# Performance work log

Measured on AMD Instinct MI355X. Metric: run time of the kernel, lower is better.

## Reference

```python
import jax, jax.numpy as jnp
import numpy as np

N = 50000
E = 500000
HID = 64
HEADS = 4
LAYERS = 4
CDIM = 8


def _p(key, shape, scale=0.05):
    return jax.random.normal(key, shape, dtype=jnp.float32) * scale


def setup_inputs() -> dict:
    key = jax.random.key(0)
    ks = jax.random.split(key, 32)
    x = jax.random.normal(ks[0], (N, 8), dtype=jnp.float32)
    src = jax.random.randint(ks[1], (E,), 0, N)
    dst = jax.random.randint(ks[2], (E,), 0, N)
    edge_index = jnp.stack([src, dst]).astype(jnp.int64)
    HC = HEADS * HID
    inp = {
        "x": x,
        "edge_index": edge_index,
        # encoder: Linear(8,64), ELU, Linear(64,64), ELU
        "enc_w1": _p(ks[3], (HID, 8)), "enc_b1": _p(ks[4], (HID,)),
        "enc_w2": _p(ks[5], (HID, HID)), "enc_b2": _p(ks[6], (HID,)),
        # per-layer TransformerConv params, stacked over layers
        "Wq": _p(ks[7], (LAYERS, HC, HID)), "bq": _p(ks[8], (LAYERS, HC)),
        "Wk": _p(ks[9], (LAYERS, HC, HID)), "bk": _p(ks[10], (LAYERS, HC)),
        "Wv": _p(ks[11], (LAYERS, HC, HID)), "bv": _p(ks[12], (LAYERS, HC)),
        "Ws": _p(ks[13], (LAYERS, HID, HID)), "bs": _p(ks[14], (LAYERS, HID)),
        # output MLP: 64->64->32->8
        "out_w1": _p(ks[15], (64, HID)), "out_b1": _p(ks[16], (64,)),
        "out_w2": _p(ks[17], (32, 64)), "out_b2": _p(ks[18], (32,)),
        "out_w3": _p(ks[19], (CDIM, 32)), "out_b3": _p(ks[20], (CDIM,)),
    }
    return inp


def transformer_conv(h, src, dst, Wq, bq, Wk, bk, Wv, bv, Ws, bs):
    """PyG TransformerConv, concat=False, root_weight=True, eval mode (no dropout)."""
    n = h.shape[0]
    q = (h @ Wq.T + bq).reshape(n, HEADS, HID)
    k = (h @ Wk.T + bk).reshape(n, HEADS, HID)
    v = (h @ Wv.T + bv).reshape(n, HEADS, HID)
    # per-edge multi-head scores: (E, H)
    alpha = jnp.einsum("ehd,ehd->eh", q[dst], k[src]) / np.sqrt(HID).astype(np.float32)
    # segment softmax over edges grouped by destination node
    amax = jax.ops.segment_max(alpha, dst, num_segments=n)          # (N, H)
    ex = jnp.exp(alpha - amax[dst])                                 # (E, H)
    denom = jax.ops.segment_sum(ex, dst, num_segments=n)           # (N, H)
    w = ex / denom[dst]                                             # (E, H)
    msg = v[src] * w[:, :, None]                                    # (E, H, C)
    agg = jax.ops.segment_sum(msg, dst, num_segments=n)            # (N, H, C)
    out = agg.mean(axis=1)                                          # concat=False -> head mean
    return out + h @ Ws.T + bs                                      # skip connection


def reference(x, edge_index, enc_w1, enc_b1, enc_w2, enc_b2,
              Wq, bq, Wk, bk, Wv, bv, Ws, bs,
              out_w1, out_b1, out_w2, out_b2, out_w3, out_b3):
    src, dst = edge_index[0], edge_index[1]
    elu = jax.nn.elu
    h = elu(x @ enc_w1.T + enc_b1)
    h = elu(h @ enc_w2.T + enc_b2)
    for l in range(LAYERS):
        h = elu(transformer_conv(h, src, dst, Wq[l], bq[l], Wk[l], bk[l],
                                 Wv[l], bv[l], Ws[l], bs[l]))
        # dropout is identity in eval mode
    o = elu(h @ out_w1.T + out_b1)
    o = elu(o @ out_w2.T + out_b2)
    o = o @ out_w3.T + out_b3
    return o
```

## Files before the change

kernel.cpp:

```cpp
#include <hip/hip_runtime.h>
#include <hip/hip_bf16.h>

#define N_NODES 50000
#define N_EDGES 500000
constexpr int HID = 64;
constexpr int HC  = 256;

typedef unsigned short u16;
typedef unsigned char u8;
typedef __attribute__((ext_vector_type(8))) __bf16 bf16x8;
typedef __attribute__((ext_vector_type(4))) float f32x4;
typedef __attribute__((ext_vector_type(2))) float f32x2;

__device__ __forceinline__ float b2f(u16 u) {
    union { unsigned int i; float f; } c; c.i = ((unsigned int)u) << 16; return c.f;
}
__device__ __forceinline__ u16 f2b(float f) {
    union { float f; unsigned int i; } c; c.f = f;
    unsigned int x = c.i;
    unsigned int lsb = (x >> 16) & 1u;
    x += 0x7fffu + lsb;
    return (u16)(x >> 16);
}
__device__ __forceinline__ float elu_f(float x) { return x > 0.f ? x : expm1f(x); }


__global__ __launch_bounds__(256) void init_kernel(int* __restrict__ cnt, int* __restrict__ cursor) {
    int i = blockIdx.x * 256 + threadIdx.x;
    if (i < N_NODES) { cnt[i] = 0; cursor[i] = 0; }
}

__global__ __launch_bounds__(256) void detect_kernel(const int* __restrict__ ei, int* __restrict__ flag) {
    __shared__ int s[4];
    int t = threadIdx.x;
    int nz = ei[2 * t + 1] != 0;
    unsigned long long m = __ballot(nz);
    if ((t & 63) == 0) s[t >> 6] = (m != 0ull) ? 1 : 0;
    __syncthreads();
    if (t == 0) flag[0] = s[0] | s[1] | s[2] | s[3];
}

__global__ __launch_bounds__(256) void hist_kernel(const int* __restrict__ ei, const int* __restrict__ flag,
                                                   int* __restrict__ cnt) {
    int e = blockIdx.x * 256 + threadIdx.x;
    if (e < N_EDGES) {
        int d = flag[0] ? ei[N_EDGES + e] : ei[2 * N_EDGES + 2 * e];
        atomicAdd(&cnt[d], 1);
    }
}

__global__ __launch_bounds__(512) void scan1_kernel(const int* __restrict__ cnt,
                                                    int* __restrict__ row_start, int* __restrict__ bsum) {
    __shared__ int sc[512];
    int t = threadIdx.x;
    int i = blockIdx.x * 512 + t;
    int v = (i < N_NODES) ? cnt[i] : 0;
    sc[t] = v;
    __syncthreads();
    for (int off = 1; off < 512; off <<= 1) {
        int u = (t >= off) ? sc[t - off] : 0;
        __syncthreads();
        sc[t] += u;
        __syncthreads();
    }
    if (i < N_NODES) row_start[i] = sc[t] - v;
    if (t == 511) bsum[blockIdx.x] = sc[511];
}

__global__ __launch_bounds__(128) void scan2_kernel(int* __restrict__ bsum, int* __restrict__ row_start) {
    __shared__ int sc[128];
    const int NB = (N_NODES + 511) / 512;
    int t = threadIdx.x;
    int v = (t < NB) ? bsum[t] : 0;
    sc[t] = v;
    __syncthreads();
    for (int off = 1; off < 128; off <<= 1) {
        int u = (t >= off) ? sc[t - off] : 0;
        __syncthreads();
        sc[t] += u;
        __syncthreads();
    }
    if (t < NB) bsum[t] = sc[t] - v;
    if (t == 127) row_start[N_NODES] = sc[127];
}

__global__ __launch_bounds__(512) void scan3_kernel(int* __restrict__ row_start, const int* __restrict__ bsum) {
    int i = blockIdx.x * 512 + threadIdx.x;
    if (i < N_NODES) row_start[i] += bsum[blockIdx.x];
}

__global__ __launch_bounds__(256) void scatter_kernel(const int* __restrict__ ei, const int* __restrict__ flag,
                                const int* __restrict__ row_start, int* __restrict__ cursor,
// ... 28 lines not shown
    }
    if (t >= 128 && t < 256) {
        int p = t - 128;
        int row = p >> 1, c = (p & 1) * 4;
        float4 val = *(const float4*)(w1 + row * 8 + c);
        *(float4*)&w1s[row * 9 + c] = val;
    }
    #pragma unroll
    for (int r = 0; r < 4; ++r) {
        int p = t + r * 256; int row = p >> 4, kc = (p & 15) * 4;
        float4 val = *(const float4*)(w2 + row * 64 + kc);
        ushort4 u; u.x = f2b(val.x); u.y = f2b(val.y); u.z = f2b(val.z); u.w = f2b(val.w);
        *(ushort4*)&w2s[row * 72 + kc] = u;
    }
    if (t < 64) { b1s[t] = b1[t]; b2s[t] = b2[t]; }
    __syncthreads();

    {
        int j = t & 63, sub = t >> 6;
        #pragma unroll
        for (int g = 0; g < 16; ++g) {
            int node = g * 4 + sub;
            float acc = b1s[j];
            #pragma unroll
            for (int m = 0; m < 8; ++m) acc += xs[node * 9 + m] * w1s[j * 9 + m];
            t1s[node * 72 + j] = f2b(elu_f(acc));
        }
    }
    __syncthreads();

    int wave = t >> 6, lane = t & 63;
    int lrow = lane & 15, quad = lane >> 4;
    int m_off = wave * 16;
    bf16x8 a0 = *(const bf16x8*)&t1s[(m_off + lrow) * 72 + quad * 8];
    bf16x8 a1 = *(const bf16x8*)&t1s[(m_off + lrow) * 72 + 32 + quad * 8];
    #pragma unroll
    for (int nsub = 0; nsub < 4; ++nsub) {
        bf16x8 b0 = *(const bf16x8*)&w2s[(nsub * 16 + lrow) * 72 + quad * 8];
        bf16x8 b1v = *(const bf16x8*)&w2s[(nsub * 16 + lrow) * 72 + 32 + quad * 8];
        f32x4 acc = {0.f, 0.f, 0.f, 0.f};
        acc = __builtin_amdgcn_mfma_f32_16x16x32_bf16(a0, b0, acc, 0, 0, 0);
        acc = __builtin_amdgcn_mfma_f32_16x16x32_bf16(a1, b1v, acc, 0, 0, 0);
        int col = nsub * 16 + lrow;
        float bias = b2s[col];
        #pragma unroll
        for (int r = 0; r < 4; ++r) {
            int row = m0 + m_off + quad * 4 + r;
            if (row < N_NODES) h[(size_t)row * 64 + col] = elu_f(acc[r] + bias);
        }
    }
}

__global__ __launch_bounds__(256) void proj_kernel(const float* __restrict__ h,
    const float* __restrict__ Wq, const float* __restrict__ bq,
    const float* __restrict__ Wk, const float* __restrict__ bk,
    const float* __restrict__ Wv, const float* __restrict__ bv,
    const float* __restrict__ Wsk, const float* __restrict__ bsk,
    int layer,
    u16* __restrict__ q, u8* __restrict__ kv,
    float* __restrict__ skip)
{
    __shared__ u16 as_tile[64 * 72];
    __shared__ u16 ws_tile[64 * 72];
    __shared__ float bias_s[64];
    __shared__ float stage[4][16 * 68];
    int t = threadIdx.x;
    int m0 = blockIdx.x * 64;

    #pragma unroll
    for (int r = 0; r < 4; ++r) {
        int p = t + r * 256; int row = p >> 4, kc = (p & 15) * 4;
        float4 val = make_float4(0.f, 0.f, 0.f, 0.f);
        if (m0 + row < N_NODES) val = *(const float4*)(h + (size_t)(m0 + row) * 64 + kc);
        ushort4 u; u.x = f2b(val.x); u.y = f2b(val.y); u.z = f2b(val.z); u.w = f2b(val.w);
        *(ushort4*)&as_tile[row * 72 + kc] = u;
    }
    __syncthreads();

    int wave = t >> 6, lane = t & 63;
    int lrow = lane & 15, quad = lane >> 4;
    int m_off = wave * 16;
    bf16x8 a0 = *(const bf16x8*)&as_tile[(m_off + lrow) * 72 + quad * 8];
    bf16x8 a1 = *(const bf16x8*)&as_tile[(m_off + lrow) * 72 + 32 + quad * 8];

    for (int ct = 0; ct < 13; ++ct) {
        const float *Wp, *bp; int cbase; int mode;
        if (ct < 4)       { Wp = Wq  + (size_t)layer * HC * HID;  bp = bq  + layer * HC;  cbase = ct * 64;       mode = 0; }
        else if (ct < 8)  { Wp = Wk  + (size_t)layer * HC * HID;  bp = bk  + layer * HC;  cbase = (ct - 4) * 64; mode = 1; }
        else if (ct < 12) { Wp = Wv  + (size_t)layer * HC * HID;  bp = bv  + layer * HC;  cbase = (ct - 8) * 64; mode = 2; }
        else              { Wp = Wsk + (size_t)layer * HID * HID; bp = bsk + layer * HID; cbase = 0;             mode = 3; }

        __syncthreads();
        #pragma unroll
        for (int r = 0; r < 4; ++r) {
            int p = t + r * 256; int row = p >> 4, kc = (p & 15) * 4;
            float4 val = *(const float4*)(Wp + (size_t)(cbase + row) * 64 + kc);
            ushort4 u; u.x = f2b(val.x); u.y = f2b(val.y); u.z = f2b(val.z); u.w = f2b(val.w);
            *(ushort4*)&ws_tile[row * 72 + kc] = u;
        }
        if (t < 64) bias_s[t] = bp[cbase + t];
        __syncthreads();

        if (mode == 1 || mode == 2) {
            #pragma unroll
            for (int nsub = 0; nsub < 4; ++nsub) {
                bf16x8 b0 = *(const bf16x8*)&ws_tile[(nsub * 16 + lrow) * 72 + quad * 8];
                bf16x8 b1 = *(const bf16x8*)&ws_tile[(nsub * 16 + lrow) * 72 + 32 + quad * 8];
                f32x4 acc = {0.f, 0.f, 0.f, 0.f};
                acc = __builtin_amdgcn_mfma_f32_16x16x32_bf16(a0, b0, acc, 0, 0, 0);
                acc = __builtin_amdgcn_mfma_f32_16x16x32_bf16(a1, b1, acc, 0, 0, 0);
                float bias = bias_s[nsub * 16 + lrow];
                #pragma unroll
                for (int r = 0; r < 4; ++r)
                    stage[wave][(quad * 4 + r) * 68 + nsub * 16 + lrow] = (acc[r] + bias) * 16.f;
            }
            int row_l = lane >> 2;
            int c0 = (lane & 3) * 16;
            int grow = m0 + m_off + row_l;
            if (grow < N_NODES) {
                const float* sp = &stage[wave][row_l * 68 + c0];
                u8* base = kv + (size_t)grow * 512 + (size_t)((cbase + c0) >> 2) * 8 + (mode == 1 ? 0 : 4);
                #pragma unroll
                for (int j = 0; j < 4; ++j) {
                    float f0 = sp[4 * j + 0], f1 = sp[4 * j + 1];
                    float f2v = sp[4 * j + 2], f3v = sp[4 * j + 3];
                    int pk = __builtin_amdgcn_cvt_pk_fp8_f32(f0, f1, 0, false);
                    pk = __builtin_amdgcn_cvt_pk_fp8_f32(f2v, f3v, pk, true);
                    *(int*)(base + j * 8) = pk;
                }
            }
        } else {
            #pragma unroll
            for (int nsub = 0; nsub < 4; ++nsub) {
                bf16x8 b0 = *(const bf16x8*)&ws_tile[(nsub * 16 + lrow) * 72 + quad * 8];
                bf16x8 b1 = *(const bf16x8*)&ws_tile[(nsub * 16 + lrow) * 72 + 32 + quad * 8];
                f32x4 acc = {0.f, 0.f, 0.f, 0.f};
                acc = __builtin_amdgcn_mfma_f32_16x16x32_bf16(a0, b0, acc, 0, 0, 0);
                acc = __builtin_amdgcn_mfma_f32_16x16x32_bf16(a1, b1, acc, 0, 0, 0);
                int col = cbase + nsub * 16 + lrow;
                float bias = bias_s[nsub * 16 + lrow];
                #pragma unroll
                for (int r = 0; r < 4; ++r) {
                    int row = m0 + m_off + quad * 4 + r;
                    if (row < N_NODES) {
                        float o = acc[r] + bias;
                        if (mode == 0) q[(size_t)row * 256 + col] = f2b(o);
                        else           skip[(size_t)row * 64 + col] = o;
                    }
                }
            }
        }
    }
}

__global__ __launch_bounds__(256) void attn_kernel(
    const u16* __restrict__ q, const u8* __restrict__ kv,
    const float* __restrict__ skip,
    const int* __restrict__ row_start, const int* __restrict__ csr_src,
    float* __restrict__ hout)
{
    int wave = threadIdx.x >> 6;
    int lane = threadIdx.x & 63;
    int n = blockIdx.x * 4 + wave;
    if (n >= N_NODES) return;
    ushort4 q4 = ((const ushort4*)(q + (size_t)n * 256))[lane];
    float qf0 = b2f(q4.x), qf1 = b2f(q4.y), qf2 = b2f(q4.z), qf3 = b2f(q4.w);
    float l = 0.f;
    float a0 = 0.f, a1 = 0.f, a2 = 0.f, a3 = 0.f;
    int e0 = row_start[n], e1 = row_start[n + 1];
    for (int e = e0; e < e1; e += 4) {
        int rem = e1 - e;
        int i1 = rem > 1 ? e + 1 : e;
        int i2 = rem > 2 ? e + 2 : e;
        int i3 = rem > 3 ? e + 3 : e;
        int s0 = csr_src[e], s1 = csr_src[i1], s2 = csr_src[i2], s3 = csr_src[i3];
        uint2 c0 = *(const uint2*)(kv + (size_t)s0 * 512 + lane * 8);
        uint2 c1 = *(const uint2*)(kv + (size_t)s1 * 512 + lane * 8);
        uint2 c2 = *(const uint2*)(kv + (size_t)s2 * 512 + lane * 8);
        uint2 c3 = *(const uint2*)(kv + (size_t)s3 * 512 + lane * 8);
        f32x2 k0a = __builtin_amdgcn_cvt_pk_f32_fp8(c0.x, false), k0b = __builtin_amdgcn_cvt_pk_f32_fp8(c0.x, true);
        f32x2 k1a = __builtin_amdgcn_cvt_pk_f32_fp8(c1.x, false), k1b = __builtin_amdgcn_cvt_pk_f32_fp8(c1.x, true);
        f32x2 k2a = __builtin_amdgcn_cvt_pk_f32_fp8(c2.x, false), k2b = __builtin_amdgcn_cvt_pk_f32_fp8(c2.x, true);
        f32x2 k3a = __builtin_amdgcn_cvt_pk_f32_fp8(c3.x, false), k3b = __builtin_amdgcn_cvt_pk_f32_fp8(c3.x, true);
        float p0 = qf0 * k0a.x + qf1 * k0a.y + qf2 * k0b.x + qf3 * k0b.y;
        float p1 = qf0 * k1a.x + qf1 * k1a.y + qf2 * k1b.x + qf3 * k1b.y;
        float p2 = qf0 * k2a.x + qf1 * k2a.y + qf2 * k2b.x + qf3 * k2b.y;
        float p3 = qf0 * k3a.x + qf1 * k3a.y + qf2 * k3b.x + qf3 * k3b.y;
        p0 += __shfl_xor(p0, 1); p1 += __shfl_xor(p1, 1); p2 += __shfl_xor(p2, 1); p3 += __shfl_xor(p3, 1);
        p0 += __shfl_xor(p0, 2); p1 += __shfl_xor(p1, 2); p2 += __shfl_xor(p2, 2); p3 += __shfl_xor(p3, 2);
        p0 += __shfl_xor(p0, 4); p1 += __shfl_xor(p1, 4); p2 += __shfl_xor(p2, 4); p3 += __shfl_xor(p3, 4);
        p0 += __shfl_xor(p0, 8); p1 += __shfl_xor(p1, 8); p2 += __shfl_xor(p2, 8); p3 += __shfl_xor(p3, 8);
        const float S = 0.0078125f;
        float w0 = __expf(p0 * S);
        float w1 = rem > 1 ? __expf(p1 * S) : 0.f;
        float w2 = rem > 2 ? __expf(p2 * S) : 0.f;
        float w3 = rem > 3 ? __expf(p3 * S) : 0.f;
        l += (w0 + w1) + (w2 + w3);
        f32x2 v0a = __builtin_amdgcn_cvt_pk_f32_fp8(c0.y, false), v0b = __builtin_amdgcn_cvt_pk_f32_fp8(c0.y, true);
        f32x2 v1a = __builtin_amdgcn_cvt_pk_f32_fp8(c1.y, false), v1b = __builtin_amdgcn_cvt_pk_f32_fp8(c1.y, true);
        f32x2 v2a = __builtin_amdgcn_cvt_pk_f32_fp8(c2.y, false), v2b = __builtin_amdgcn_cvt_pk_f32_fp8(c2.y, true);
        f32x2 v3a = __builtin_amdgcn_cvt_pk_f32_fp8(c3.y, false), v3b = __builtin_amdgcn_cvt_pk_f32_fp8(c3.y, true);
        a0 += w0 * v0a.x + w1 * v1a.x + w2 * v2a.x + w3 * v3a.x;
        a1 += w0 * v0a.y + w1 * v1a.y + w2 * v2a.y + w3 * v3a.y;
        a2 += w0 * v0b.x + w1 * v1b.x + w2 * v2b.x + w3 * v3b.x;
        a3 += w0 * v0b.y + w1 * v1b.y + w2 * v2b.y + w3 * v3b.y;
    }
    float inv = l > 0.f ? 1.f / l : 0.f;
    a0 *= inv; a1 *= inv; a2 *= inv; a3 *= inv;
    a0 += __shfl_xor(a0, 16); a0 += __shfl_xor(a0, 32);
    a1 += __shfl_xor(a1, 16); a1 += __shfl_xor(a1, 32);
    a2 += __shfl_xor(a2, 16); a2 += __shfl_xor(a2, 32);
    a3 += __shfl_xor(a3, 16); a3 += __shfl_xor(a3, 32);
    if ((lane >> 4) == 0) {
        const float OS = 0.015625f;
        float4 sk = ((const float4*)(skip + (size_t)n * 64))[lane];
        float4 o;
        o.x = elu_f(OS * a0 + sk.x);
        o.y = elu_f(OS * a1 + sk.y);
        o.z = elu_f(OS * a2 + sk.z);
        o.w = elu_f(OS * a3 + sk.w);
        ((float4*)(hout + (size_t)n * 64))[lane] = o;
    }
}

__global__ __launch_bounds__(256) void mlp_kernel(const float* __restrict__ h,
    const float* __restrict__ w1, const float* __restrict__ b1,
    const float* __restrict__ w2, const float* __restrict__ b2,
    const float* __restrict__ w3, const float* __restrict__ b3,
    float* __restrict__ out)
{
    __shared__ u16 hs[64 * 72];
    __shared__ u16 w1s[64 * 72];
    __shared__ u16 t1s[64 * 72];
    __shared__ u16 w2s[32 * 72];
    __shared__ float t2s[64 * 33];
    __shared__ float w3s[8 * 33];
    __shared__ float b1s[64], b2s[32], b3s[8];
    int t = threadIdx.x;
    int m0 = blockIdx.x * 64;

    #pragma unroll
    for (int r = 0; r < 4; ++r) {
        int p = t + r * 256; int row = p >> 4, kc = (p & 15) * 4;
        float4 val = make_float4(0.f, 0.f, 0.f, 0.f);
        if (m0 + row < N_NODES) val = *(const float4*)(h + (size_t)(m0 + row) * 64 + kc);
        ushort4 u; u.x = f2b(val.x); u.y = f2b(val.y); u.z = f2b(val.z); u.w = f2b(val.w);
        *(ushort4*)&hs[row * 72 + kc] = u;
    }
    #pragma unroll
    for (int r = 0; r < 4; ++r) {
        int p = t + r * 256; int row = p >> 4, kc = (p & 15) * 4;
        float4 val = *(const float4*)(w1 + row * 64 + kc);
        ushort4 u; u.x = f2b(val.x); u.y = f2b(val.y); u.z = f2b(val.z); u.w = f2b(val.w);
        *(ushort4*)&w1s[row * 72 + kc] = u;
    }
    #pragma unroll
    for (int r = 0; r < 2; ++r) {
        int p = t + r * 256; int row = p >> 4, kc = (p & 15) * 4;
// ... 54 lines not shown
    __syncthreads();

    #pragma unroll
    for (int r = 0; r < 2; ++r) {
        int idx = t + r * 256;
        int node = idx >> 3, j = idx & 7;
        int row = m0 + node;
        if (row < N_NODES) {
            float acc = b3s[j];
            #pragma unroll
            for (int kk = 0; kk < 32; ++kk) acc += t2s[node * 33 + kk] * w3s[j * 33 + kk];
            out[(size_t)row * 8 + j] = acc;
        }
    }
}

extern "C" void kernel_launch(void* const* d_in, const int* in_sizes, int n_in,
                              void* d_out, int out_size, void* d_ws, size_t ws_size,
                              hipStream_t stream) {
    (void)in_sizes; (void)n_in; (void)out_size; (void)ws_size;
    const float* x   = (const float*)d_in[0];
    const int* ei    = (const int*)d_in[1];
    const float* ew1 = (const float*)d_in[2];
    const float* eb1 = (const float*)d_in[3];
    const float* ew2 = (const float*)d_in[4];
    const float* eb2 = (const float*)d_in[5];
    const float* Wq  = (const float*)d_in[6];
    const float* bq  = (const float*)d_in[7];
    const float* Wk  = (const float*)d_in[8];
    const float* bk  = (const float*)d_in[9];
    const float* Wv  = (const float*)d_in[10];
    const float* bv  = (const float*)d_in[11];
    const float* Wsk = (const float*)d_in[12];
    const float* bsk = (const float*)d_in[13];
    const float* ow1 = (const float*)d_in[14];
    const float* ob1 = (const float*)d_in[15];
    const float* ow2 = (const float*)d_in[16];
    const float* ob2 = (const float*)d_in[17];
    const float* ow3 = (const float*)d_in[18];
    const float* ob3 = (const float*)d_in[19];

    char* ws = (char*)d_ws;
    size_t off = 0;
    auto alloc = [&](size_t bytes) -> void* {
        void* p = ws + off;
        off += (bytes + 255) & ~(size_t)255;
        return p;
    };
    float* h0    = (float*)alloc((size_t)N_NODES * 64 * 4);
    float* h1    = (float*)alloc((size_t)N_NODES * 64 * 4);
    u16*   q     = (u16*)  alloc((size_t)N_NODES * 256 * 2);
    u8*    kv    = (u8*)   alloc((size_t)N_NODES * 512);
    float* skp   = (float*)alloc((size_t)N_NODES * 64 * 4);
    int*   cnt   = (int*)  alloc((size_t)N_NODES * 4);
    int*   cursor= (int*)  alloc((size_t)N_NODES * 4);
    int*   rowst = (int*)  alloc((size_t)(N_NODES + 1) * 4);
    int*   csr   = (int*)  alloc((size_t)N_EDGES * 4);
    int*   bsum  = (int*)  alloc(512);
    int*   flag  = (int*)  alloc(256);

    const int NB = (N_NODES + 511) / 512;

    init_kernel<<<(N_NODES + 255) / 256, 256, 0, stream>>>(cnt, cursor);
    detect_kernel<<<1, 256, 0, stream>>>(ei, flag);
    hist_kernel<<<(N_EDGES + 255) / 256, 256, 0, stream>>>(ei, flag, cnt);
    scan1_kernel<<<NB, 512, 0, stream>>>(cnt, rowst, bsum);
    scan2_kernel<<<1, 128, 0, stream>>>(bsum, rowst);
    scan3_kernel<<<NB, 512, 0, stream>>>(rowst, bsum);
    scatter_kernel<<<(N_EDGES + 255) / 256, 256, 0, stream>>>(ei, flag, rowst, cursor, csr);

    encoder_kernel<<<(N_NODES + 63) / 64, 256, 0, stream>>>(x, ew1, eb1, ew2, eb2, h0);

    float* hin = h0;
    float* hout = h1;
    for (int l = 0; l < 4; ++l) {
        proj_kernel<<<(N_NODES + 63) / 64, 256, 0, stream>>>(hin, Wq, bq, Wk, bk, Wv, bv, Wsk, bsk, l, q, kv, skp);
        attn_kernel<<<(N_NODES + 3) / 4, 256, 0, stream>>>(q, kv, skp, rowst, csr, hout);
        float* tmp = hin; hin = hout; hout = tmp;
    }

    mlp_kernel<<<(N_NODES + 63) / 64, 256, 0, stream>>>(hin, ow1, ob1, ow2, ob2, ow3, ob3, (float*)d_out);
}
```

Baseline: 520.6 us.

## Pre-convert weights to bf16, stage projection outputs in LDS, unroll attention gather by 8

A one-time kernel converts the Q/K/V/skip weights to bf16, so the projection kernel reads MFMA B fragments straight from global memory instead of reconverting the fp32 weights into LDS in every block. Projection outputs are staged through a shared LDS pool and written with coalesced 16-byte stores, with K and V interleaved into the packed fp8 layout. The attention loop processes 8 edges per iteration instead of 4, giving more gathers in flight. The cost is extra register pressure in the attention kernel and uncached global fragment loads of the weights.

```diff
diff --git a/kernel.cpp b/kernel.cpp
--- a/kernel.cpp
+++ b/kernel.cpp
@@ -38,6 +38,21 @@
     if ((t & 63) == 0) s[t >> 6] = (m != 0ull) ? 1 : 0;
     __syncthreads();
     if (t == 0) flag[0] = s[0] | s[1] | s[2] | s[3];
+}
+
+__global__ __launch_bounds__(256) void wcvt_kernel(const float* __restrict__ Wq, const float* __restrict__ Wk,
+                                                   const float* __restrict__ Wv, const float* __restrict__ Wsk,
+                                                   u16* __restrict__ w16) {
+    int i = blockIdx.x * 256 + threadIdx.x;
+    if (i >= 53248) return;
+    const float* src; int off;
+    if (i < 16384)      { src = Wq;  off = i; }
+    else if (i < 32768) { src = Wk;  off = i - 16384; }
+    else if (i < 49152) { src = Wv;  off = i - 32768; }
+    else                { src = Wsk; off = i - 49152; }
+    float4 v = ((const float4*)src)[off];
+    ushort4 u; u.x = f2b(v.x); u.y = f2b(v.y); u.z = f2b(v.z); u.w = f2b(v.w);
+    ((ushort4*)w16)[i] = u;
 }
 
 __global__ __launch_bounds__(256) void hist_kernel(const int* __restrict__ ei, const int* __restrict__ flag,
@@ -172,18 +187,21 @@
 }
 
 __global__ __launch_bounds__(256) void proj_kernel(const float* __restrict__ h,
-    const float* __restrict__ Wq, const float* __restrict__ bq,
-    const float* __restrict__ Wk, const float* __restrict__ bk,
-    const float* __restrict__ Wv, const float* __restrict__ bv,
-    const float* __restrict__ Wsk, const float* __restrict__ bsk,
+    const u16* __restrict__ wq16, const u16* __restrict__ wk16,
+    const u16* __restrict__ wv16, const u16* __restrict__ wsk16,
+    const float* __restrict__ bq, const float* __restrict__ bk,
+    const float* __restrict__ bv, const float* __restrict__ bsk,
     int layer,
-    u16* __restrict__ q, u8* __restrict__ kv,
-    float* __restrict__ skip)
+    u16* __restrict__ q, u8* __restrict__ kv, float* __restrict__ skip)
 {
     __shared__ u16 as_tile[64 * 72];
-    __shared__ u16 ws_tile[64 * 72];
+    __shared__ float poolf[4352];
     __shared__ float bias_s[64];
-    __shared__ float stage[4][16 * 68];
+    __shared__ float bias_s2[64];
+    u16* ot_h = (u16*)poolf;
+    u8*  kbuf = (u8*)poolf;
+    u8*  vbuf = (u8*)poolf + 4608;
+
     int t = threadIdx.x;
     int m0 = blockIdx.x * 64;
 
@@ -203,72 +221,117 @@
     bf16x8 a0 = *(const bf16x8*)&as_tile[(m_off + lrow) * 72 + quad * 8];
     bf16x8 a1 = *(const bf16x8*)&as_tile[(m_off + lrow) * 72 + 32 + quad * 8];
 
-    for (int ct = 0; ct < 13; ++ct) {
-        const float *Wp, *bp; int cbase; int mode;
-        if (ct < 4)       { Wp = Wq  + (size_t)layer * HC * HID;  bp = bq  + layer * HC;  cbase = ct * 64;       mode = 0; }
-        else if (ct < 8)  { Wp = Wk  + (size_t)layer * HC * HID;  bp = bk  + layer * HC;  cbase = (ct - 4) * 64; mode = 1; }
-        else if (ct < 12) { Wp = Wv  + (size_t)layer * HC * HID;  bp = bv  + layer * HC;  cbase = (ct - 8) * 64; mode = 2; }
-        else              { Wp = Wsk + (size_t)layer * HID * HID; bp = bsk + layer * HID; cbase = 0;             mode = 3; }
-
-        __syncthreads();
-        #pragma unroll
-        for (int r = 0; r < 4; ++r) {
-            int p = t + r * 256; int row = p >> 4, kc = (p & 15) * 4;
-            float4 val = *(const float4*)(Wp + (size_t)(cbase + row) * 64 + kc);
-            ushort4 u; u.x = f2b(val.x); u.y = f2b(val.y); u.z = f2b(val.z); u.w = f2b(val.w);
-            *(ushort4*)&ws_tile[row * 72 + kc] = u;
-        }
-        if (t < 64) bias_s[t] = bp[cbase + t];
-        __syncthreads();
-
-        if (mode == 1 || mode == 2) {
-            #pragma unroll
-            for (int nsub = 0; nsub < 4; ++nsub) {
-                bf16x8 b0 = *(const bf16x8*)&ws_tile[(nsub * 16 + lrow) * 72 + quad * 8];
-                bf16x8 b1 = *(const bf16x8*)&ws_tile[(nsub * 16 + lrow) * 72 + 32 + quad * 8];
-                f32x4 acc = {0.f, 0.f, 0.f, 0.f};
-                acc = __builtin_amdgcn_mfma_f32_16x16x32_bf16(a0, b0, acc, 0, 0, 0);
-                acc = __builtin_amdgcn_mfma_f32_16x16x32_bf16(a1, b1, acc, 0, 0, 0);
-                float bias = bias_s[nsub * 16 + lrow];
-                #pragma unroll
-                for (int r = 0; r < 4; ++r)
-                    stage[wave][(quad * 4 + r) * 68 + nsub * 16 + lrow] = (acc[r] + bias) * 16.f;
+    const u16* Wq16  = wq16  + (size_t)layer * HC * HID;
+    const u16* Wk16  = wk16  + (size_t)layer * HC * HID;
+    const u16* Wv16  = wv16  + (size_t)layer * HC * HID;
+    const u16* Wsk16 = wsk16 + (size_t)layer * HID * HID;
+
+    for (int ct = 0; ct < 4; ++ct) {
+        int cbase = ct * 64;
+        if (t < 64) bias_s[t] = bq[layer * HC + cbase + t];
+        __syncthreads();
+        #pragma unroll
+        for (int nsub = 0; nsub < 4; ++nsub) {
+            const u16* wrow = Wq16 + (size_t)(cbase + nsub * 16 + lrow) * 64 + quad * 8;
+            bf16x8 b0 = *(const bf16x8*)wrow;
+            bf16x8 b1 = *(const bf16x8*)(wrow + 32);
+            f32x4 acc = {0.f, 0.f, 0.f, 0.f};
+            acc = __builtin_amdgcn_mfma_f32_16x16x32_bf16(a0, b0, acc, 0, 0, 0);
+            acc = __builtin_amdgcn_mfma_f32_16x16x32_bf16(a1, b1, acc, 0, 0, 0);
+            float bias = bias_s[nsub * 16 + lrow];
+            #pragma unroll
+            for (int r = 0; r < 4; ++r)
+                ot_h[(m_off + quad * 4 + r) * 72 + nsub * 16 + lrow] = f2b(acc[r] + bias);
+        }
+        __syncthreads();
+        #pragma unroll
+        for (int it = 0; it < 2; ++it) {
+            int p = t + it * 256; int row = p >> 3, ch = p & 7;
+            int grow = m0 + row;
+            if (grow < N_NODES) {
+                uint4 val = *(const uint4*)&ot_h[row * 72 + ch * 8];
+                *(uint4*)(q + (size_t)grow * 256 + cbase + ch * 8) = val;
             }
-            int row_l = lane >> 2;
-            int c0 = (lane & 3) * 16;
-            int grow = m0 + m_off + row_l;
+        }
+    }
+
+    for (int ct = 0; ct < 4; ++ct) {
+        int cbase = ct * 64;
+        if (t < 64) bias_s[t] = bk[layer * HC + cbase + t];
+        else if (t < 128) bias_s2[t - 64] = bv[layer * HC + cbase + (t - 64)];
+        __syncthreads();
+        #pragma unroll
+        for (int nsub = 0; nsub < 4; ++nsub) {
+            const u16* wrow = Wk16 + (size_t)(cbase + nsub * 16 + lrow) * 64 + quad * 8;
+            bf16x8 b0 = *(const bf16x8*)wrow;
+            bf16x8 b1 = *(const bf16x8*)(wrow + 32);
+            f32x4 acc = {0.f, 0.f, 0.f, 0.f};
+            acc = __builtin_amdgcn_mfma_f32_16x16x32_bf16(a0, b0, acc, 0, 0, 0);
+            acc = __builtin_amdgcn_mfma_f32_16x16x32_bf16(a1, b1, acc, 0, 0, 0);
+            float bias = bias_s[nsub * 16 + lrow];
+            #pragma unroll
+            for (int r = 0; r < 4; ++r) {
+                float f = (acc[r] + bias) * 16.f;
+                int pk = __builtin_amdgcn_cvt_pk_fp8_f32(f, f, 0, false);
+                kbuf[(m_off + quad * 4 + r) * 72 + nsub * 16 + lrow] = (u8)(pk & 0xff);
+            }
+        }
+        #pragma unroll
+        for (int nsub = 0; nsub < 4; ++nsub) {
+            const u16* wrow = Wv16 + (size_t)(cbase + nsub * 16 + lrow) * 64 + quad * 8;
+            bf16x8 b0 = *(const bf16x8*)wrow;
+            bf16x8 b1 = *(const bf16x8*)(wrow + 32);
+            f32x4 acc = {0.f, 0.f, 0.f, 0.f};
+            acc = __builtin_amdgcn_mfma_f32_16x16x32_bf16(a0, b0, acc, 0, 0, 0);
+            acc = __builtin_amdgcn_mfma_f32_16x16x32_bf16(a1, b1, acc, 0, 0, 0);
+            float bias = bias_s2[nsub * 16 + lrow];
+            #pragma unroll
+            for (int r = 0; r < 4; ++r) {
+                float f = (acc[r] + bias) * 16.f;
+                int pk = __builtin_amdgcn_cvt_pk_fp8_f32(f, f, 0, false);
+                vbuf[(m_off + quad * 4 + r) * 72 + nsub * 16 + lrow] = (u8)(pk & 0xff);
+            }
+        }
+        __syncthreads();
+        #pragma unroll
+        for (int it = 0; it < 2; ++it) {
+            int p = t + it * 256; int row = p >> 3, ch = p & 7;
+            int grow = m0 + row;
             if (grow < N_NODES) {
-                const float* sp = &stage[wave][row_l * 68 + c0];
-                u8* base = kv + (size_t)grow * 512 + (size_t)((cbase + c0) >> 2) * 8 + (mode == 1 ? 0 : 4);
-                #pragma unroll
-                for (int j = 0; j < 4; ++j) {
-                    float f0 = sp[4 * j + 0], f1 = sp[4 * j + 1];
-                    float f2v = sp[4 * j + 2], f3v = sp[4 * j + 3];
-                    int pk = __builtin_amdgcn_cvt_pk_fp8_f32(f0, f1, 0, false);
-                    pk = __builtin_amdgcn_cvt_pk_fp8_f32(f2v, f3v, pk, true);
-                    *(int*)(base + j * 8) = pk;
-                }
+                unsigned int k01 = *(const unsigned int*)&kbuf[row * 72 + ch * 8];
+                unsigned int k23 = *(const unsigned int*)&kbuf[row * 72 + ch * 8 + 4];
+                unsigned int v01 = *(const unsigned int*)&vbuf[row * 72 + ch * 8];
+                unsigned int v23 = *(const unsigned int*)&vbuf[row * 72 + ch * 8 + 4];
+                uint4 val; val.x = k01; val.y = v01; val.z = k23; val.w = v23;
+                *(uint4*)(kv + (size_t)grow * 512 + cbase * 2 + ch * 16) = val;
             }
-        } else {
-            #pragma unroll
-            for (int nsub = 0; nsub < 4; ++nsub) {
-                bf16x8 b0 = *(const bf16x8*)&ws_tile[(nsub * 16 + lrow) * 72 + quad * 8];
-                bf16x8 b1 = *(const bf16x8*)&ws_tile[(nsub * 16 + lrow) * 72 + 32 + quad * 8];
-                f32x4 acc = {0.f, 0.f, 0.f, 0.f};
-                acc = __builtin_amdgcn_mfma_f32_16x16x32_bf16(a0, b0, acc, 0, 0, 0);
-                acc = __builtin_amdgcn_mfma_f32_16x16x32_bf16(a1, b1, acc, 0, 0, 0);
-                int col = cbase + nsub * 16 + lrow;
-                float bias = bias_s[nsub * 16 + lrow];
-                #pragma unroll
-                for (int r = 0; r < 4; ++r) {
-                    int row = m0 + m_off + quad * 4 + r;
-                    if (row < N_NODES) {
-                        float o = acc[r] + bias;
-                        if (mode == 0) q[(size_t)row * 256 + col] = f2b(o);
-                        else           skip[(size_t)row * 64 + col] = o;
-                    }
-                }
-            }
+        }
+    }
+
+    {
+        float* ot_f = poolf;
+        if (t < 64) bias_s[t] = bsk[layer * HID + t];
+        __syncthreads();
+        #pragma unroll
+        for (int nsub = 0; nsub < 4; ++nsub) {
+            const u16* wrow = Wsk16 + (size_t)(nsub * 16 + lrow) * 64 + quad * 8;
+            bf16x8 b0 = *(const bf16x8*)wrow;
+            bf16x8 b1 = *(const bf16x8*)(wrow + 32);
+            f32x4 acc = {0.f, 0.f, 0.f, 0.f};
+            acc = __builtin_amdgcn_mfma_f32_16x16x32_bf16(a0, b0, acc, 0, 0, 0);
+            acc = __builtin_amdgcn_mfma_f32_16x16x32_bf16(a1, b1, acc, 0, 0, 0);
+            float bias = bias_s[nsub * 16 + lrow];
+            #pragma unroll
+            for (int r = 0; r < 4; ++r)
+                ot_f[(m_off + quad * 4 + r) * 68 + nsub * 16 + lrow] = acc[r] + bias;
+        }
+        __syncthreads();
+        int row = t >> 2, c4 = (t & 3) * 16;
+        int grow = m0 + row;
+        if (grow < N_NODES) {
+            #pragma unroll
+            for (int j = 0; j < 4; ++j)
+                *(float4*)(skip + (size_t)grow * 64 + c4 + j * 4) = *(const float4*)&ot_f[row * 68 + c4 + j * 4];
         }
     }
 }
@@ -285,45 +348,52 @@
     if (n >= N_NODES) return;
     ushort4 q4 = ((const ushort4*)(q + (size_t)n * 256))[lane];
     float qf0 = b2f(q4.x), qf1 = b2f(q4.y), qf2 = b2f(q4.z), qf3 = b2f(q4.w);
+    const u8* kvl = kv + lane * 8;
     float l = 0.f;
     float a0 = 0.f, a1 = 0.f, a2 = 0.f, a3 = 0.f;
     int e0 = row_start[n], e1 = row_start[n + 1];
-    for (int e = e0; e < e1; e += 4) {
+    for (int e = e0; e < e1; e += 8) {
         int rem = e1 - e;
-        int i1 = rem > 1 ? e + 1 : e;
-        int i2 = rem > 2 ? e + 2 : e;
-        int i3 = rem > 3 ? e + 3 : e;
-        int s0 = csr_src[e], s1 = csr_src[i1], s2 = csr_src[i2], s3 = csr_src[i3];
-        uint2 c0 = *(const uint2*)(kv + (size_t)s0 * 512 + lane * 8);
-        uint2 c1 = *(const uint2*)(kv + (size_t)s1 * 512 + lane * 8);
-        uint2 c2 = *(const uint2*)(kv + (size_t)s2 * 512 + lane * 8);
-        uint2 c3 = *(const uint2*)(kv + (size_t)s3 * 512 + lane * 8);
-        f32x2 k0a = __builtin_amdgcn_cvt_pk_f32_fp8(c0.x, false), k0b = __builtin_amdgcn_cvt_pk_f32_fp8(c0.x, true);
-        f32x2 k1a = __builtin_amdgcn_cvt_pk_f32_fp8(c1.x, false), k1b = __builtin_amdgcn_cvt_pk_f32_fp8(c1.x, true);
-        f32x2 k2a = __builtin_amdgcn_cvt_pk_f32_fp8(c2.x, false), k2b = __builtin_amdgcn_cvt_pk_f32_fp8(c2.x, true);
-        f32x2 k3a = __builtin_amdgcn_cvt_pk_f32_fp8(c3.x, false), k3b = __builtin_amdgcn_cvt_pk_f32_fp8(c3.x, true);
-        float p0 = qf0 * k0a.x + qf1 * k0a.y + qf2 * k0b.x + qf3 * k0b.y;
-        float p1 = qf0 * k1a.x + qf1 * k1a.y + qf2 * k1b.x + qf3 * k1b.y;
-        float p2 = qf0 * k2a.x + qf1 * k2a.y + qf2 * k2b.x + qf3 * k2b.y;
-        float p3 = qf0 * k3a.x + qf1 * k3a.y + qf2 * k3b.x + qf3 * k3b.y;
-        p0 += __shfl_xor(p0, 1); p1 += __shfl_xor(p1, 1); p2 += __shfl_xor(p2, 1); p3 += __shfl_xor(p3, 1);
-        p0 += __shfl_xor(p0, 2); p1 += __shfl_xor(p1, 2); p2 += __shfl_xor(p2, 2); p3 += __shfl_xor(p3, 2);
-        p0 += __shfl_xor(p0, 4); p1 += __shfl_xor(p1, 4); p2 += __shfl_xor(p2, 4); p3 += __shfl_xor(p3, 4);
-        p0 += __shfl_xor(p0, 8); p1 += __shfl_xor(p1, 8); p2 += __shfl_xor(p2, 8); p3 += __shfl_xor(p3, 8);
+        int s[8];
+        #pragma unroll
+        for (int j = 0; j < 8; ++j) {
+            int jj = j < rem ? j : rem - 1;
+            s[j] = csr_src[e + jj];
+        }
+        uint2 c[8];
+        #pragma unroll
+        for (int j = 0; j < 8; ++j) c[j] = *(const uint2*)(kvl + (size_t)s[j] * 512);
+        float p[8];
+        #pragma unroll
+        for (int j = 0; j < 8; ++j) {
+            f32x2 ka = __builtin_amdgcn_cvt_pk_f32_fp8(c[j].x, false);
+            f32x2 kb = __builtin_amdgcn_cvt_pk_f32_fp8(c[j].x, true);
+            p[j] = qf0 * ka.x + qf1 * ka.y + qf2 * kb.x + qf3 * kb.y;
+        }
+        #pragma unroll
+        for (int j = 0; j < 8; ++j) p[j] += __shfl_xor(p[j], 1);
+        #pragma unroll
+        for (int j = 0; j < 8; ++j) p[j] += __shfl_xor(p[j], 2);
+        #pragma unroll
+        for (int j = 0; j < 8; ++j) p[j] += __shfl_xor(p[j], 4);
+        #pragma unroll
+        for (int j = 0; j < 8; ++j) p[j] += __shfl_xor(p[j], 8);
         const float S = 0.0078125f;
-        float w0 = __expf(p0 * S);
-        float w1 = rem > 1 ? __expf(p1 * S) : 0.f;
-        float w2 = rem > 2 ? __expf(p2 * S) : 0.f;
-        float w3 = rem > 3 ? __expf(p3 * S) : 0.f;
-        l += (w0 + w1) + (w2 + w3);
-        f32x2 v0a = __builtin_amdgcn_cvt_pk_f32_fp8(c0.y, false), v0b = __builtin_amdgcn_cvt_pk_f32_fp8(c0.y, true);
-        f32x2 v1a = __builtin_amdgcn_cvt_pk_f32_fp8(c1.y, false), v1b = __builtin_amdgcn_cvt_pk_f32_fp8(c1.y, true);
-        f32x2 v2a = __builtin_amdgcn_cvt_pk_f32_fp8(c2.y, false), v2b = __builtin_amdgcn_cvt_pk_f32_fp8(c2.y, true);
-        f32x2 v3a = __builtin_amdgcn_cvt_pk_f32_fp8(c3.y, false), v3b = __builtin_amdgcn_cvt_pk_f32_fp8(c3.y, true);
-        a0 += w0 * v0a.x + w1 * v1a.x + w2 * v2a.x + w3 * v3a.x;
-        a1 += w0 * v0a.y + w1 * v1a.y + w2 * v2a.y + w3 * v3a.y;
-        a2 += w0 * v0b.x + w1 * v1b.x + w2 * v2b.x + w3 * v3b.x;
-        a3 += w0 * v0b.y + w1 * v1b.y + w2 * v2b.y + w3 * v3b.y;
+        float w[8];
+        w[0] = __expf(p[0] * S);
+        #pragma unroll
+        for (int j = 1; j < 8; ++j) w[j] = j < rem ? __expf(p[j] * S) : 0.f;
+        float ls = 0.f;
+        #pragma unroll
+        for (int j = 0; j < 8; ++j) ls += w[j];
+        l += ls;
+        #pragma unroll
+        for (int j = 0; j < 8; ++j) {
+            f32x2 va = __builtin_amdgcn_cvt_pk_f32_fp8(c[j].y, false);
+            f32x2 vb = __builtin_amdgcn_cvt_pk_f32_fp8(c[j].y, true);
+            a0 += w[j] * va.x; a1 += w[j] * va.y;
+            a2 += w[j] * vb.x; a3 += w[j] * vb.y;
+        }
     }
     float inv = l > 0.f ? 1.f / l : 0.f;
     a0 *= inv; a1 *= inv; a2 *= inv; a3 *= inv;
@@ -484,6 +554,7 @@
     u16*   q     = (u16*)  alloc((size_t)N_NODES * 256 * 2);
     u8*    kv    = (u8*)   alloc((size_t)N_NODES * 512);
     float* skp   = (float*)alloc((size_t)N_NODES * 64 * 4);
+    u16*   w16   = (u16*)  alloc((size_t)212992 * 2);
     int*   cnt   = (int*)  alloc((size_t)N_NODES * 4);
     int*   cursor= (int*)  alloc((size_t)N_NODES * 4);
     int*   rowst = (int*)  alloc((size_t)(N_NODES + 1) * 4);
@@ -491,10 +562,16 @@
     int*   bsum  = (int*)  alloc(512);
     int*   flag  = (int*)  alloc(256);
 
+    u16* wq16  = w16;
+    u16* wk16  = w16 + 65536;
+    u16* wv16  = w16 + 131072;
+    u16* wsk16 = w16 + 196608;
+
     const int NB = (N_NODES + 511) / 512;
 
     init_kernel<<<(N_NODES + 255) / 256, 256, 0, stream>>>(cnt, cursor);
     detect_kernel<<<1, 256, 0, stream>>>(ei, flag);
+    wcvt_kernel<<<208, 256, 0, stream>>>(Wq, Wk, Wv, Wsk, w16);
     hist_kernel<<<(N_EDGES + 255) / 256, 256, 0, stream>>>(ei, flag, cnt);
     scan1_kernel<<<NB, 512, 0, stream>>>(cnt, rowst, bsum);
     scan2_kernel<<<1, 128, 0, stream>>>(bsum, rowst);
@@ -506,7 +583,8 @@
     float* hin = h0;
     float* hout = h1;
     for (int l = 0; l < 4; ++l) {
-        proj_kernel<<<(N_NODES + 63) / 64, 256, 0, stream>>>(hin, Wq, bq, Wk, bk, Wv, bv, Wsk, bsk, l, q, kv, skp);
+        proj_kernel<<<(N_NODES + 63) / 64, 256, 0, stream>>>(hin, wq16, wk16, wv16, wsk16,
+                                                             bq, bk, bv, bsk, l, q, kv, skp);
         attn_kernel<<<(N_NODES + 3) / 4, 256, 0, stream>>>(q, kv, skp, rowst, csr, hout);
         float* tmp = hin; hin = hout; hout = tmp;
     }
```

Result: slower. 614.3 us (+18.0%).

## Pre-convert projection weights to bf16 and stage outputs for coalesced stores

Applied to the files above, without the earlier changes.

Adds a one-time kernel that converts Wq/Wk/Wv/Ws to bf16, so each proj block loads bf16 weights directly instead of converting fp32 per block. The MFMA operands are swapped so each lane holds 4 consecutive output columns. Results for q, the packed fp8 k/v and skip are staged in a shared pool and written to global memory with 16-byte coalesced stores instead of scattered 2- and 4-byte stores. This adds extra barriers and one extra launch.

```diff
diff --git a/kernel.cpp b/kernel.cpp
--- a/kernel.cpp
+++ b/kernel.cpp
@@ -38,6 +38,21 @@
     if ((t & 63) == 0) s[t >> 6] = (m != 0ull) ? 1 : 0;
     __syncthreads();
     if (t == 0) flag[0] = s[0] | s[1] | s[2] | s[3];
+}
+
+__global__ __launch_bounds__(256) void wcvt_kernel(const float* __restrict__ Wq, const float* __restrict__ Wk,
+                                                   const float* __restrict__ Wv, const float* __restrict__ Wsk,
+                                                   u16* __restrict__ w16) {
+    int i = blockIdx.x * 256 + threadIdx.x;
+    if (i >= 53248) return;
+    const float* src; int off;
+    if (i < 16384)      { src = Wq;  off = i; }
+    else if (i < 32768) { src = Wk;  off = i - 16384; }
+    else if (i < 49152) { src = Wv;  off = i - 32768; }
+    else                { src = Wsk; off = i - 49152; }
+    float4 v = ((const float4*)src)[off];
+    ushort4 u; u.x = f2b(v.x); u.y = f2b(v.y); u.z = f2b(v.z); u.w = f2b(v.w);
+    ((ushort4*)w16)[i] = u;
 }
 
 __global__ __launch_bounds__(256) void hist_kernel(const int* __restrict__ ei, const int* __restrict__ flag,
@@ -172,18 +187,20 @@
 }
 
 __global__ __launch_bounds__(256) void proj_kernel(const float* __restrict__ h,
-    const float* __restrict__ Wq, const float* __restrict__ bq,
-    const float* __restrict__ Wk, const float* __restrict__ bk,
-    const float* __restrict__ Wv, const float* __restrict__ bv,
-    const float* __restrict__ Wsk, const float* __restrict__ bsk,
+    const u16* __restrict__ wq16, const u16* __restrict__ wk16,
+    const u16* __restrict__ wv16, const u16* __restrict__ wsk16,
+    const float* __restrict__ bq, const float* __restrict__ bk,
+    const float* __restrict__ bv, const float* __restrict__ bsk,
     int layer,
-    u16* __restrict__ q, u8* __restrict__ kv,
-    float* __restrict__ skip)
+    u16* __restrict__ q, u8* __restrict__ kv, float* __restrict__ skip)
 {
     __shared__ u16 as_tile[64 * 72];
     __shared__ u16 ws_tile[64 * 72];
-    __shared__ float bias_s[64];
-    __shared__ float stage[4][16 * 68];
+    __shared__ float pool[64 * 68];
+    u16* qst  = (u16*)pool;
+    u8*  kvst = (u8*)pool;
+    float* skst = pool;
+
     int t = threadIdx.x;
     int m0 = blockIdx.x * 64;
 
@@ -199,76 +216,137 @@
 
     int wave = t >> 6, lane = t & 63;
     int lrow = lane & 15, quad = lane >> 4;
-    int m_off = wave * 16;
-    bf16x8 a0 = *(const bf16x8*)&as_tile[(m_off + lrow) * 72 + quad * 8];
-    bf16x8 a1 = *(const bf16x8*)&as_tile[(m_off + lrow) * 72 + 32 + quad * 8];
-
-    for (int ct = 0; ct < 13; ++ct) {
-        const float *Wp, *bp; int cbase; int mode;
-        if (ct < 4)       { Wp = Wq  + (size_t)layer * HC * HID;  bp = bq  + layer * HC;  cbase = ct * 64;       mode = 0; }
-        else if (ct < 8)  { Wp = Wk  + (size_t)layer * HC * HID;  bp = bk  + layer * HC;  cbase = (ct - 4) * 64; mode = 1; }
-        else if (ct < 12) { Wp = Wv  + (size_t)layer * HC * HID;  bp = bv  + layer * HC;  cbase = (ct - 8) * 64; mode = 2; }
-        else              { Wp = Wsk + (size_t)layer * HID * HID; bp = bsk + layer * HID; cbase = 0;             mode = 3; }
-
-        __syncthreads();
-        #pragma unroll
-        for (int r = 0; r < 4; ++r) {
-            int p = t + r * 256; int row = p >> 4, kc = (p & 15) * 4;
-            float4 val = *(const float4*)(Wp + (size_t)(cbase + row) * 64 + kc);
-            ushort4 u; u.x = f2b(val.x); u.y = f2b(val.y); u.z = f2b(val.z); u.w = f2b(val.w);
-            *(ushort4*)&ws_tile[row * 72 + kc] = u;
-        }
-        if (t < 64) bias_s[t] = bp[cbase + t];
-        __syncthreads();
-
-        if (mode == 1 || mode == 2) {
+    bf16x8 a0 = *(const bf16x8*)&as_tile[(wave * 16 + lrow) * 72 + quad * 8];
+    bf16x8 a1 = *(const bf16x8*)&as_tile[(wave * 16 + lrow) * 72 + 32 + quad * 8];
+
+    const u16* Wq16  = wq16  + (size_t)layer * HC * HID;
+    const u16* Wk16  = wk16  + (size_t)layer * HC * HID;
+    const u16* Wv16  = wv16  + (size_t)layer * HC * HID;
+    const u16* Wsk16 = wsk16 + (size_t)layer * HID * HID;
+    const float* bqL  = bq  + layer * HC;
+    const float* bkL  = bk  + layer * HC;
+    const float* bvL  = bv  + layer * HC;
+    const float* bskL = bsk + layer * HID;
+
+    int nl = wave * 16 + lrow;
+    int grow_l = m0 + nl;
+
+    for (int ct = 0; ct < 4; ++ct) {
+        int cbase = ct * 64;
+        __syncthreads();
+        #pragma unroll
+        for (int it = 0; it < 2; ++it) {
+            int p = t + it * 256; int row = p >> 3, kc = (p & 7) * 8;
+            *(uint4*)&ws_tile[row * 72 + kc] = *(const uint4*)(Wq16 + (size_t)(cbase + row) * 64 + kc);
+        }
+        __syncthreads();
+        #pragma unroll
+        for (int nsub = 0; nsub < 4; ++nsub) {
+            bf16x8 w0 = *(const bf16x8*)&ws_tile[(nsub * 16 + lrow) * 72 + quad * 8];
+            bf16x8 w1 = *(const bf16x8*)&ws_tile[(nsub * 16 + lrow) * 72 + 32 + quad * 8];
+            f32x4 acc = {0.f, 0.f, 0.f, 0.f};
+            acc = __builtin_amdgcn_mfma_f32_16x16x32_bf16(w0, a0, acc, 0, 0, 0);
+            acc = __builtin_amdgcn_mfma_f32_16x16x32_bf16(w1, a1, acc, 0, 0, 0);
+            float4 b4 = *(const float4*)(bqL + cbase + nsub * 16 + quad * 4);
+            ushort4 o;
+            o.x = f2b(acc[0] + b4.x); o.y = f2b(acc[1] + b4.y);
+            o.z = f2b(acc[2] + b4.z); o.w = f2b(acc[3] + b4.w);
+            *(ushort4*)&qst[nl * 72 + nsub * 16 + quad * 4] = o;
+        }
+        __syncthreads();
+        #pragma unroll
+        for (int it = 0; it < 2; ++it) {
+            int p = t + it * 256; int row = p >> 3, ch = p & 7;
+            int grow = m0 + row;
+            if (grow < N_NODES)
+                *(uint4*)(q + (size_t)grow * 256 + cbase + ch * 8) = *(const uint4*)&qst[row * 72 + ch * 8];
+        }
+    }
+
+    for (int ct = 0; ct < 4; ++ct) {
+        int cbase = ct * 64;
+        __syncthreads();
+        #pragma unroll
+        for (int it = 0; it < 2; ++it) {
+            int p = t + it * 256; int row = p >> 3, kc = (p & 7) * 8;
+            *(uint4*)&ws_tile[row * 72 + kc] = *(const uint4*)(Wk16 + (size_t)(cbase + row) * 64 + kc);
+        }
+        __syncthreads();
+        #pragma unroll
+        for (int nsub = 0; nsub < 4; ++nsub) {
+            bf16x8 w0 = *(const bf16x8*)&ws_tile[(nsub * 16 + lrow) * 72 + quad * 8];
+            bf16x8 w1 = *(const bf16x8*)&ws_tile[(nsub * 16 + lrow) * 72 + 32 + quad * 8];
+            f32x4 acc = {0.f, 0.f, 0.f, 0.f};
+            acc = __builtin_amdgcn_mfma_f32_16x16x32_bf16(w0, a0, acc, 0, 0, 0);
+            acc = __builtin_amdgcn_mfma_f32_16x16x32_bf16(w1, a1, acc, 0, 0, 0);
+            float4 b4 = *(const float4*)(bkL + cbase + nsub * 16 + quad * 4);
+            float f0 = (acc[0] + b4.x) * 16.f, f1 = (acc[1] + b4.y) * 16.f;
+            float f2v = (acc[2] + b4.z) * 16.f, f3v = (acc[3] + b4.w) * 16.f;
+            int pk = __builtin_amdgcn_cvt_pk_fp8_f32(f0, f1, 0, false);
+            pk = __builtin_amdgcn_cvt_pk_fp8_f32(f2v, f3v, pk, true);
+            int g = nsub * 4 + quad;
+            *(unsigned int*)&kvst[nl * 144 + g * 8] = (unsigned int)pk;
+        }
+        __syncthreads();
+        #pragma unroll
+        for (int it = 0; it < 2; ++it) {
+            int p = t + it * 256; int row = p >> 3, kc = (p & 7) * 8;
+            *(uint4*)&ws_tile[row * 72 + kc] = *(const uint4*)(Wv16 + (size_t)(cbase + row) * 64 + kc);
+        }
+        __syncthreads();
+        #pragma unroll
+        for (int nsub = 0; nsub < 4; ++nsub) {
+            bf16x8 w0 = *(const bf16x8*)&ws_tile[(nsub * 16 + lrow) * 72 + quad * 8];
+            bf16x8 w1 = *(const bf16x8*)&ws_tile[(nsub * 16 + lrow) * 72 + 32 + quad * 8];
+            f32x4 acc = {0.f, 0.f, 0.f, 0.f};
+            acc = __builtin_amdgcn_mfma_f32_16x16x32_bf16(w0, a0, acc, 0, 0, 0);
+            acc = __builtin_amdgcn_mfma_f32_16x16x32_bf16(w1, a1, acc, 0, 0, 0);
+            float4 b4 = *(const float4*)(bvL + cbase + nsub * 16 + quad * 4);
+            float f0 = (acc[0] + b4.x) * 16.f, f1 = (acc[1] + b4.y) * 16.f;
+            float f2v = (acc[2] + b4.z) * 16.f, f3v = (acc[3] + b4.w) * 16.f;
+            int pk = __builtin_amdgcn_cvt_pk_fp8_f32(f0, f1, 0, false);
+            pk = __builtin_amdgcn_cvt_pk_fp8_f32(f2v, f3v, pk, true);
+            int g = nsub * 4 + quad;
+            *(unsigned int*)&kvst[nl * 144 + g * 8 + 4] = (unsigned int)pk;
+        }
+        __syncthreads();
+        #pragma unroll
+        for (int it = 0; it < 2; ++it) {
+            int p = t + it * 256; int row = p >> 3, ch = p & 7;
+            int grow = m0 + row;
+            if (grow < N_NODES)
+                *(uint4*)(kv + (size_t)grow * 512 + cbase * 2 + ch * 16) = *(const uint4*)&kvst[row * 144 + ch * 16];
+        }
+    }
+
+    {
+        __syncthreads();
+        #pragma unroll
+        for (int it = 0; it < 2; ++it) {
+            int p = t + it * 256; int row = p >> 3, kc = (p & 7) * 8;
+            *(uint4*)&ws_tile[row * 72 + kc] = *(const uint4*)(Wsk16 + (size_t)row * 64 + kc);
+        }
+        __syncthreads();
+        #pragma unroll
+        for (int nsub = 0; nsub < 4; ++nsub) {
+            bf16x8 w0 = *(const bf16x8*)&ws_tile[(nsub * 16 + lrow) * 72 + quad * 8];
+            bf16x8 w1 = *(const bf16x8*)&ws_tile[(nsub * 16 + lrow) * 72 + 32 + quad * 8];
+            f32x4 acc = {0.f, 0.f, 0.f, 0.f};
+            acc = __builtin_amdgcn_mfma_f32_16x16x32_bf16(w0, a0, acc, 0, 0, 0);
+            acc = __builtin_amdgcn_mfma_f32_16x16x32_bf16(w1, a1, acc, 0, 0, 0);
+            float4 b4 = *(const float4*)(bskL + nsub * 16 + quad * 4);
+            float4 o;
+            o.x = acc[0] + b4.x; o.y = acc[1] + b4.y;
+            o.z = acc[2] + b4.z; o.w = acc[3] + b4.w;
+            *(float4*)&skst[nl * 68 + nsub * 16 + quad * 4] = o;
+        }
+        __syncthreads();
+        int row = t >> 2, c0 = (t & 3) * 16;
+        int grow = m0 + row;
+        if (grow < N_NODES) {
             #pragma unroll
-            for (int nsub = 0; nsub < 4; ++nsub) {
-                bf16x8 b0 = *(const bf16x8*)&ws_tile[(nsub * 16 + lrow) * 72 + quad * 8];
-                bf16x8 b1 = *(const bf16x8*)&ws_tile[(nsub * 16 + lrow) * 72 + 32 + quad * 8];
-                f32x4 acc = {0.f, 0.f, 0.f, 0.f};
-                acc = __builtin_amdgcn_mfma_f32_16x16x32_bf16(a0, b0, acc, 0, 0, 0);
-                acc = __builtin_amdgcn_mfma_f32_16x16x32_bf16(a1, b1, acc, 0, 0, 0);
-                float bias = bias_s[nsub * 16 + lrow];
-                #pragma unroll
-                for (int r = 0; r < 4; ++r)
-                    stage[wave][(quad * 4 + r) * 68 + nsub * 16 + lrow] = (acc[r] + bias) * 16.f;
-            }
-            int row_l = lane >> 2;
-            int c0 = (lane & 3) * 16;
-            int grow = m0 + m_off + row_l;
-            if (grow < N_NODES) {
-                const float* sp = &stage[wave][row_l * 68 + c0];
-                u8* base = kv + (size_t)grow * 512 + (size_t)((cbase + c0) >> 2) * 8 + (mode == 1 ? 0 : 4);
-                #pragma unroll
-                for (int j = 0; j < 4; ++j) {
-                    float f0 = sp[4 * j + 0], f1 = sp[4 * j + 1];
-                    float f2v = sp[4 * j + 2], f3v = sp[4 * j + 3];
-                    int pk = __builtin_amdgcn_cvt_pk_fp8_f32(f0, f1, 0, false);
-                    pk = __builtin_amdgcn_cvt_pk_fp8_f32(f2v, f3v, pk, true);
-                    *(int*)(base + j * 8) = pk;
-                }
-            }
-        } else {
-            #pragma unroll
-            for (int nsub = 0; nsub < 4; ++nsub) {
-                bf16x8 b0 = *(const bf16x8*)&ws_tile[(nsub * 16 + lrow) * 72 + quad * 8];
-                bf16x8 b1 = *(const bf16x8*)&ws_tile[(nsub * 16 + lrow) * 72 + 32 + quad * 8];
-                f32x4 acc = {0.f, 0.f, 0.f, 0.f};
-                acc = __builtin_amdgcn_mfma_f32_16x16x32_bf16(a0, b0, acc, 0, 0, 0);
-                acc = __builtin_amdgcn_mfma_f32_16x16x32_bf16(a1, b1, acc, 0, 0, 0);
-                int col = cbase + nsub * 16 + lrow;
-                float bias = bias_s[nsub * 16 + lrow];
-                #pragma unroll
-                for (int r = 0; r < 4; ++r) {
-                    int row = m0 + m_off + quad * 4 + r;
-                    if (row < N_NODES) {
-                        float o = acc[r] + bias;
-                        if (mode == 0) q[(size_t)row * 256 + col] = f2b(o);
-                        else           skip[(size_t)row * 64 + col] = o;
-                    }
-                }
-            }
+            for (int j = 0; j < 4; ++j)
+                *(float4*)(skip + (size_t)grow * 64 + c0 + j * 4) = *(const float4*)&skst[row * 68 + c0 + j * 4];
         }
     }
 }
@@ -285,6 +363,7 @@
     if (n >= N_NODES) return;
     ushort4 q4 = ((const ushort4*)(q + (size_t)n * 256))[lane];
     float qf0 = b2f(q4.x), qf1 = b2f(q4.y), qf2 = b2f(q4.z), qf3 = b2f(q4.w);
+    const u8* kvl = kv + lane * 8;
     float l = 0.f;
     float a0 = 0.f, a1 = 0.f, a2 = 0.f, a3 = 0.f;
     int e0 = row_start[n], e1 = row_start[n + 1];
@@ -294,10 +373,10 @@
         int i2 = rem > 2 ? e + 2 : e;
         int i3 = rem > 3 ? e + 3 : e;
         int s0 = csr_src[e], s1 = csr_src[i1], s2 = csr_src[i2], s3 = csr_src[i3];
-        uint2 c0 = *(const uint2*)(kv + (size_t)s0 * 512 + lane * 8);
-        uint2 c1 = *(const uint2*)(kv + (size_t)s1 * 512 + lane * 8);
-        uint2 c2 = *(const uint2*)(kv + (size_t)s2 * 512 + lane * 8);
-        uint2 c3 = *(const uint2*)(kv + (size_t)s3 * 512 + lane * 8);
+        uint2 c0 = *(const uint2*)(kvl + (size_t)s0 * 512);
+        uint2 c1 = *(const uint2*)(kvl + (size_t)s1 * 512);
+        uint2 c2 = *(const uint2*)(kvl + (size_t)s2 * 512);
+        uint2 c3 = *(const uint2*)(kvl + (size_t)s3 * 512);
         f32x2 k0a = __builtin_amdgcn_cvt_pk_f32_fp8(c0.x, false), k0b = __builtin_amdgcn_cvt_pk_f32_fp8(c0.x, true);
         f32x2 k1a = __builtin_amdgcn_cvt_pk_f32_fp8(c1.x, false), k1b = __builtin_amdgcn_cvt_pk_f32_fp8(c1.x, true);
         f32x2 k2a = __builtin_amdgcn_cvt_pk_f32_fp8(c2.x, false), k2b = __builtin_amdgcn_cvt_pk_f32_fp8(c2.x, true);
@@ -484,6 +563,7 @@
     u16*   q     = (u16*)  alloc((size_t)N_NODES * 256 * 2);
     u8*    kv    = (u8*)   alloc((size_t)N_NODES * 512);
     float* skp   = (float*)alloc((size_t)N_NODES * 64 * 4);
+    u16*   w16   = (u16*)  alloc((size_t)212992 * 2);
     int*   cnt   = (int*)  alloc((size_t)N_NODES * 4);
     int*   cursor= (int*)  alloc((size_t)N_NODES * 4);
     int*   rowst = (int*)  alloc((size_t)(N_NODES + 1) * 4);
@@ -491,10 +571,16 @@
     int*   bsum  = (int*)  alloc(512);
     int*   flag  = (int*)  alloc(256);
 
+    u16* wq16  = w16;
+    u16* wk16  = w16 + 65536;
+    u16* wv16  = w16 + 131072;
+    u16* wsk16 = w16 + 196608;
+
     const int NB = (N_NODES + 511) / 512;
 
     init_kernel<<<(N_NODES + 255) / 256, 256, 0, stream>>>(cnt, cursor);
     detect_kernel<<<1, 256, 0, stream>>>(ei, flag);
+    wcvt_kernel<<<208, 256, 0, stream>>>(Wq, Wk, Wv, Wsk, w16);
     hist_kernel<<<(N_EDGES + 255) / 256, 256, 0, stream>>>(ei, flag, cnt);
     scan1_kernel<<<NB, 512, 0, stream>>>(cnt, rowst, bsum);
     scan2_kernel<<<1, 128, 0, stream>>>(bsum, rowst);
@@ -506,7 +592,8 @@
     float* hin = h0;
     float* hout = h1;
     for (int l = 0; l < 4; ++l) {
-        proj_kernel<<<(N_NODES + 63) / 64, 256, 0, stream>>>(hin, Wq, bq, Wk, bk, Wv, bv, Wsk, bsk, l, q, kv, skp);
+        proj_kernel<<<(N_NODES + 63) / 64, 256, 0, stream>>>(hin, wq16, wk16, wv16, wsk16,
+                                                             bq, bk, bv, bsk, l, q, kv, skp);
         attn_kernel<<<(N_NODES + 3) / 4, 256, 0, stream>>>(q, kv, skp, rowst, csr, hout);
         float* tmp = hin; hin = hout; hout = tmp;
     }
```

Result: faster. 471.5 us (-9.4%).
